# Optimization experiments

Measured on AMD Instinct MI355X. Metric: run time of the kernel, lower is better.

Reference implementation:

```python
import jax, jax.numpy as jnp
import numpy as np

B, N, K, H = 32, 1024, 10, 64  # graphs, nodes per graph, kNN, hidden_channels


def setup_inputs() -> dict:
    key = jax.random.key(0)
    ks = jax.random.split(key, 11)
    def w(k, shape, fan_in):
        lim = 1.0 / np.sqrt(fan_in)
        return jax.random.uniform(k, shape, jnp.float32, -lim, lim)
    return {
        'pos': jax.random.uniform(ks[0], (B, N, 2), jnp.float32),  # TSP city coords
        'W1': w(ks[1], (4, H), 4),           'b1': w(ks[2], (H,), 4),
        'W2': w(ks[3], (2 * H, 2 * H), 2 * H), 'b2': w(ks[4], (2 * H,), 2 * H),
        'W3': w(ks[5], (4 * H, 4 * H), 4 * H), 'b3': w(ks[6], (4 * H,), 4 * H),
        'Wl1': w(ks[7], (4 * H, H), 4 * H),   'bl1': w(ks[8], (H,), 4 * H),
        'Wl2': w(ks[9], (H, 2), H),           'bl2': w(ks[10], (2,), H),
    }


def _edge_conv(x, W, b, k):
    # DynamicEdgeConv: kNN graph in feature space (self-match included, as in
    # torch_cluster.knn(x, x, k)), edge feature [x_i, x_j - x_i], Linear, max-aggr.
    sq = jnp.sum(x * x, axis=-1)                                   # [B,N]
    dist = sq[:, :, None] + sq[:, None, :] - 2.0 * jnp.einsum('bnd,bmd->bnm', x, x)
    _, idx = jax.lax.top_k(-dist, k)                               # [B,N,k]
    xj = jax.vmap(lambda xb, ib: xb[ib])(x, idx)                   # [B,N,k,D]
    xi = x[:, :, None, :]
    edge = jnp.concatenate([jnp.broadcast_to(xi, xj.shape), xj - xi], axis=-1)
    msg = edge @ W + b                                             # [B,N,k,Dout]
    return jnp.max(msg, axis=2)                                    # max aggregation


def _pair_norm(x, eps=1e-5, scale=1.0):
    # PairNorm over all nodes (module calls it without batch vector)
    xc = x - jnp.mean(x, axis=(0, 1), keepdims=True)
    msn = jnp.mean(jnp.sum(xc * xc, axis=-1))  # mean squared node norm
    return scale * xc / jnp.sqrt(eps + msn)


def reference(pos, W1, b1, W2, b2, W3, b3, Wl1, bl1, Wl2, bl2):
    h1 = _pair_norm(jax.nn.relu(_edge_conv(pos, W1, b1, K)))
    h2 = _pair_norm(jax.nn.relu(_edge_conv(h1, W2, b2, K)))
    h3 = _pair_norm(jax.nn.relu(_edge_conv(h2, W3, b3, K)))
    g = jnp.max(h3, axis=1)                    # global_max_pool per graph -> [B,4H]
    h = jax.nn.relu(g @ Wl1 + bl1)             # dropout(p=0.2) is identity in eval
    return h @ Wl2 + bl2                       # [B,2]
```

## Files before the change

kernel.cpp:

```cpp
#include <hip/hip_runtime.h>
#include <math.h>

constexpr int NB = 32;
constexpr int NP = 1024;
constexpr int NK = 10;
constexpr int BN = NB * NP;
constexpr int NBCH = 8;
constexpr int NSLOT = 1024;

__device__ __forceinline__ float4 ld4(const float* p){ return *reinterpret_cast<const float4*>(p); }
__device__ __forceinline__ float2 ld2(const float* p){ return *reinterpret_cast<const float2*>(p); }
__device__ __forceinline__ void st4(float* p, float4 v){ *reinterpret_cast<float4*>(p) = v; }

__global__ __launch_bounds__(256) void k_sq_pos(const float* __restrict__ x, float* __restrict__ sq){
  int i = blockIdx.x*256 + threadIdx.x;
  float2 v = ld2(x + (size_t)2*i);
  sq[i] = v.x*v.x + v.y*v.y;
}

__global__ __launch_bounds__(256) void k_dist2(const float* __restrict__ x,
    const float* __restrict__ sq, float* __restrict__ dist, int b0){
  int bz = blockIdx.z;
  int b = b0 + bz;
  int n0 = blockIdx.x*128, m0 = blockIdx.y*128;
  int ry = threadIdx.x>>4, rx = threadIdx.x&15;
  const float* xb = x + (size_t)b*NP*2;
  const float* sqb = sq + (size_t)b*NP;
  float2 av[8], bv[8]; float sn[8], sm[8];
#pragma unroll
  for (int k=0;k<8;++k){
    av[k] = ld2(xb + (size_t)(n0+ry*8+k)*2);
    bv[k] = ld2(xb + (size_t)(m0+rx*8+k)*2);
    sn[k] = sqb[n0+ry*8+k];
    sm[k] = sqb[m0+rx*8+k];
  }
  float* dbase = dist + ((size_t)bz*NP + n0 + ry*8)*NP + m0 + rx*8;
#pragma unroll
  for (int k=0;k<8;++k){
    float r[8];
#pragma unroll
    for (int l=0;l<8;++l){
      float dot = av[k].x*bv[l].x + av[k].y*bv[l].y;
      r[l] = (sn[k] + sm[l]) - 2.f*dot;
    }
    st4(dbase + (size_t)k*NP,     make_float4(r[0],r[1],r[2],r[3]));
    st4(dbase + (size_t)k*NP + 4, make_float4(r[4],r[5],r[6],r[7]));
  }
}

template<int DIN>
__global__ __launch_bounds__(256) void k_dist(const float* __restrict__ x,
    const float* __restrict__ sq, float* __restrict__ dist, int b0){
  constexpr int K4 = DIN/4, MASK = K4-1;
  extern __shared__ float4 smem[];
  float4* as4 = smem;
  float4* bs4 = smem + 128*K4;
  int bz = blockIdx.z;
  int b = b0 + bz;
  int n0 = blockIdx.x*128, m0 = blockIdx.y*128;
  int ry = threadIdx.x>>4, rx = threadIdx.x&15;
  const float* xb = x + (size_t)b*NP*DIN;
  for (int u=threadIdx.x; u<128*K4; u+=256){
    int r = u / K4, c = u % K4;
    int sw = r*K4 + ((c + (r>>3)) & MASK);
    as4[sw] = ld4(xb + (size_t)(n0+r)*DIN + 4*c);
    bs4[sw] = ld4(xb + (size_t)(m0+r)*DIN + 4*c);
  }
  __syncthreads();
  float acc[8][8];
#pragma unroll
  for (int k=0;k<8;++k)
#pragma unroll
    for (int l=0;l<8;++l) acc[k][l] = 0.f;
#pragma unroll 2
  for (int d4=0; d4<K4; ++d4){
    float4 a_[8], b_[8];
#pragma unroll
    for (int k=0;k<8;++k) a_[k] = as4[(ry*8+k)*K4 + ((d4 + ry) & MASK)];
#pragma unroll
    for (int l=0;l<8;++l) b_[l] = bs4[(rx*8+l)*K4 + ((d4 + rx) & MASK)];
#pragma unroll
    for (int k=0;k<8;++k)
#pragma unroll
      for (int l=0;l<8;++l)
        acc[k][l] += a_[k].x*b_[l].x + a_[k].y*b_[l].y + a_[k].z*b_[l].z + a_[k].w*b_[l].w;
  }
  const float* sqb = sq + (size_t)b*NP;
  float sn[8], sm[8];
#pragma unroll
  for (int k=0;k<8;++k){ sn[k] = sqb[n0+ry*8+k]; sm[k] = sqb[m0+rx*8+k]; }
  float* dbase = dist + ((size_t)bz*NP + n0 + ry*8)*NP + m0 + rx*8;
#pragma unroll
  for (int k=0;k<8;++k){
    float r[8];
#pragma unroll
    for (int l=0;l<8;++l) r[l] = (sn[k]+sm[l]) - 2.f*acc[k][l];
    st4(dbase + (size_t)k*NP,     make_float4(r[0],r[1],r[2],r[3]));
    st4(dbase + (size_t)k*NP + 4, make_float4(r[4],r[5],r[6],r[7]));
  }
}

template<int DIN, int DOUT>
__global__ __launch_bounds__(256) void k_gemm(const float* __restrict__ x,
    const float* __restrict__ W, float* __restrict__ xcat, int m_base){
  constexpr int K4 = DIN/4, MASK = K4-1;
  extern __shared__ float4 smem[];
  float4* as4 = smem;
  float4* bs4 = smem + 128*K4;
  int m0 = blockIdx.x*128;
  int nc = blockIdx.y*128;
  bool isBot = (nc >= DOUT);
  int bcol = isBot ? nc - DOUT : nc;
  const float* B = W + (isBot ? (size_t)DIN*DOUT : 0);
  const float* xg = x + (size_t)(m_base + m0)*DIN;
  for (int u=threadIdx.x; u<128*K4; u+=256){
    int r = u / K4, c = u % K4;
    as4[r*K4 + ((c + (r>>3)) & MASK)] = ld4(xg + (size_t)r*DIN + 4*c);
  }
  float* bsf = reinterpret_cast<float*>(bs4);
  for (int u=threadIdx.x; u<DIN*128; u+=256){
    int k = u >> 7, n = u & 127;
    bsf[(n*K4 + (((k>>2) + (n>>3)) & MASK))*4 + (k&3)] = B[(size_t)k*DOUT + bcol + n];
  }
  __syncthreads();
  int ry = threadIdx.x>>4, rx = threadIdx.x&15;
  float acc[8][8];
#pragma unroll
  for (int k=0;k<8;++k)
#pragma unroll
    for (int l=0;l<8;++l) acc[k][l] = 0.f;
#pragma unroll 2
  for (int d4=0; d4<K4; ++d4){
    float4 a_[8], b_[8];
#pragma unroll
    for (int k=0;k<8;++k) a_[k] = as4[(ry*8+k)*K4 + ((d4 + ry) & MASK)];
#pragma unroll
    for (int l=0;l<8;++l) b_[l] = bs4[(rx*8+l)*K4 + ((d4 + rx) & MASK)];
#pragma unroll
    for (int k=0;k<8;++k)
#pragma unroll
      for (int l=0;l<8;++l)
        acc[k][l] += a_[k].x*b_[l].x + a_[k].y*b_[l].y + a_[k].z*b_[l].z + a_[k].w*b_[l].w;
  }
  float* outb = xcat + (size_t)(m0 + ry*8)*(2*DOUT) + nc + rx*8;
#pragma unroll
  for (int k=0;k<8;++k){
    st4(outb + (size_t)k*(2*DOUT),     make_float4(acc[k][0],acc[k][1],acc[k][2],acc[k][3]));
    st4(outb + (size_t)k*(2*DOUT) + 4, make_float4(acc[k][4],acc[k][5],acc[k][6],acc[k][7]));
  }
}

template<int DOUT>
__global__ __launch_bounds__(256) void k_gmax(const float* __restrict__ xcat,
    const int* __restrict__ idx, const float* __restrict__ bias,
    float* __restrict__ hout, float* __restrict__ spart, int p_base, int slot_base){
  constexpr int TP = DOUT/4;
  constexpr int ROWS = 256/TP;
  constexpr int PPT = 32/ROWS;
  __shared__ int idx_s[32*NK];
  __shared__ float red[1024];
  __shared__ float ssp[4];
  int c4 = threadIdx.x % TP, pr = threadIdx.x / TP;
  int c = 4*c4;
  int p0 = blockIdx.x*32 + p_base;
  for (int t=threadIdx.x; t<32*NK; t+=256) idx_s[t] = idx[(size_t)p0*NK + t];
  __syncthreads();
  float4 b4 = ld4(bias + c);
  float4 fsum = make_float4(0.f,0.f,0.f,0.f);
  float ss = 0.f;
  int pbl = (((p0 - p_base) >> 10) << 10);
#pragma unroll
  for (int t=0; t<PPT; ++t){
    int pl = pr + t*ROWS;
    int lrow = (p0 - p_base) + pl;
    const float* row = xcat + (size_t)lrow*(2*DOUT);
    float4 z = ld4(row + c), ys = ld4(row + DOUT + c);
    float4 mv = make_float4(-__builtin_inff(),-__builtin_inff(),-__builtin_inff(),-__builtin_inff());
    for (int j=0;j<NK;++j){
      int q = pbl + idx_s[pl*NK + j];
      float4 g = ld4(xcat + (size_t)q*(2*DOUT) + DOUT + c);
      mv.x = fmaxf(mv.x, g.x); mv.y = fmaxf(mv.y, g.y);
      mv.z = fmaxf(mv.z, g.z); mv.w = fmaxf(mv.w, g.w);
    }
    float4 v;
    v.x = fmaxf(z.x + b4.x - ys.x + mv.x, 0.f);
    v.y = fmaxf(z.y + b4.y - ys.y + mv.y, 0.f);
    v.z = fmaxf(z.z + b4.z - ys.z + mv.z, 0.f);
    v.w = fmaxf(z.w + b4.w - ys.w + mv.w, 0.f);
    st4(hout + (size_t)(p0 + pl)*DOUT + c, v);
    fsum.x += v.x; fsum.y += v.y; fsum.z += v.z; fsum.w += v.w;
    ss += v.x*v.x + v.y*v.y + v.z*v.z + v.w*v.w;
  }
  st4(&red[pr*DOUT + c], fsum);
#pragma unroll
  for (int off=32; off; off>>=1) ss += __shfl_xor(ss, off, 64);
  if ((threadIdx.x&63)==0) ssp[threadIdx.x>>6] = ss;
  __syncthreads();
  int slot = slot_base + blockIdx.x;
  for (int o=threadIdx.x; o<DOUT; o+=256){
    float s = 0.f;
#pragma unroll
    for (int r=0;r<ROWS;++r) s += red[r*DOUT + o];
    spart[(size_t)o*NSLOT + slot] = s;
  }
  if (threadIdx.x==0) spart[(size_t)DOUT*NSLOT + slot] = ssp[0]+ssp[1]+ssp[2]+ssp[3];
}

__global__ __launch_bounds__(256) void k_topk(const float* __restrict__ dist,
    int* __restrict__ idx, int b0){
  int wave = threadIdx.x>>6, lane = threadIdx.x&63;
  int rowg = blockIdx.x*4 + wave;
  int bz = rowg >> 10, n = rowg & 1023;
  const float* dr = dist + (size_t)rowg * NP;
  float dv[16];
#pragma unroll
  for (int t=0;t<16;++t) dv[t] = dr[lane + 64*t];
  int* out = idx + ((size_t)(b0+bz)*NP + n)*NK;
  for (int kk=0; kk<NK; ++kk){
    float bvv = dv[0]; int bm = lane;
#pragma unroll
    for (int t=1;t<16;++t){
      int m = lane + 64*t;
      if (dv[t] < bvv){ bvv = dv[t]; bm = m; }
    }
#pragma unroll
    for (int off=32; off; off>>=1){
      float ov = __shfl_xor(bvv, off, 64);
      int om = __shfl_xor(bm, off, 64);
      if (ov < bvv || (ov == bvv && om < bm)){ bvv = ov; bm = om; }
    }
    if (lane == 0) out[kk] = bm;
    int tsel = bm>>6, lsel = bm&63;
#pragma unroll
    for (int t=0;t<16;++t)
      if (t == tsel && lane == lsel) dv[t] = __builtin_inff();
  }
}

__global__ __launch_bounds__(256) void k_edge1(const float* __restrict__ x,
    const int* __restrict__ idx, const float* __restrict__ W,
    const float* __restrict__ bias, float* __restrict__ hout,
    float* __restrict__ spart){
  __shared__ int idx_s[32*NK];
  __shared__ float red[4][64];
  __shared__ float ssw[4];
  int lane = threadIdx.x & 63, wv = threadIdx.x >> 6;
  int p0 = blockIdx.x * 32;
  int b = p0 >> 10;
  int pl0 = p0 & 1023;
  const float* xb = x + ((size_t)b<<10)*2;
  for (int t=threadIdx.x; t<32*NK; t+=256) idx_s[t] = idx[(size_t)p0*NK + t];
  __syncthreads();
  float w0=W[lane], w1=W[64+lane], w2=W[128+lane], w3=W[192+lane];
  float bi = bias[lane];
  float fsum = 0.f, ss = 0.f;
#pragma unroll
  for (int t=0;t<8;++t){
    int pl = wv*8 + t;
    float2 xi = ld2(xb + (size_t)(pl0+pl)*2);
    float common = xi.x*w0 + xi.y*w1 + bi;
    float mv = -__builtin_inff();
    for (int j=0;j<NK;++j){
      float2 xj = ld2(xb + (size_t)idx_s[pl*NK+j]*2);
      mv = fmaxf(mv, (xj.x-xi.x)*w2 + (xj.y-xi.y)*w3);
    }
    float v = fmaxf(common + mv, 0.f);
    hout[(size_t)(p0+pl)*64 + lane] = v;
    fsum += v; ss += v*v;
  }
  red[wv][lane] = fsum;
#pragma unroll
  for (int off=32; off; off>>=1) ss += __shfl_xor(ss, off, 64);
  if (lane==0) ssw[wv] = ss;
  __syncthreads();
  if (threadIdx.x < 64){
    float s = red[0][lane]+red[1][lane]+red[2][lane]+red[3][lane];
    spart[(size_t)lane*NSLOT + blockIdx.x] = s;
  }
  if (threadIdx.x==0) spart[(size_t)64*NSLOT + blockIdx.x] = ssw[0]+ssw[1]+ssw[2]+ssw[3];
}

template<int DOUT>
__global__ __launch_bounds__(256) void k_finalize2(const float* __restrict__ spart,
    float* __restrict__ stats){
  __shared__ float part[4];
  __shared__ float ssh;
  float musq = 0.f;
  for (int f = threadIdx.x; f <= DOUT; f += 256){
    const float* row = spart + (size_t)f*NSLOT;
    float4 a = make_float4(0.f,0.f,0.f,0.f);
    for (int s=0; s<NSLOT; s+=4){
      float4 v = ld4(row + s);
      a.x += v.x; a.y += v.y; a.z += v.z; a.w += v.w;
    }
    float s = (a.x + a.y) + (a.z + a.w);
    if (f < DOUT){
      float m = s * (1.f/BN);
      stats[320+f] = m;
      musq += m*m;
    } else {
      ssh = s;
    }
  }
#pragma unroll
  for (int off=32; off; off>>=1) musq += __shfl_xor(musq, off, 64);
  if ((threadIdx.x&63)==0) part[threadIdx.x>>6] = musq;
  __syncthreads();
  if (threadIdx.x==0){
    float mu2 = part[0]+part[1]+part[2]+part[3];
    float msn = ssh*(1.f/BN) - mu2;
    stats[576] = 1.f / sqrtf(1e-5f + msn);
  }
}

template<int DOUT>
__global__ __launch_bounds__(256) void k_norm(float* __restrict__ h,
    const float* __restrict__ stats, float* __restrict__ sq){
  int lane = threadIdx.x&63, wv = threadIdx.x>>6;
  int row = blockIdx.x*4 + wv;
  float inv = stats[576];
  const float* mu = stats + 320;
  float* hr = h + (size_t)row*DOUT;
  float s = 0.f;
  if constexpr (DOUT == 64){
    float v = (hr[lane] - mu[lane]) * inv;
    hr[lane] = v;
    s = v*v;
  } else if constexpr (DOUT == 128){
    float2 x2 = ld2(hr + 2*lane), m2 = ld2(mu + 2*lane);
    float a = (x2.x - m2.x)*inv, b = (x2.y - m2.y)*inv;
    *reinterpret_cast<float2*>(hr + 2*lane) = make_float2(a,b);
    s = a*a + b*b;
  } else {
    float4 x4 = ld4(hr + 4*lane), m4 = ld4(mu + 4*lane);
    float4 v;
    v.x = (x4.x-m4.x)*inv; v.y = (x4.y-m4.y)*inv;
    v.z = (x4.z-m4.z)*inv; v.w = (x4.w-m4.w)*inv;
    st4(hr + 4*lane, v);
    s = v.x*v.x + v.y*v.y + v.z*v.z + v.w*v.w;
  }
#pragma unroll
  for (int off=32; off; off>>=1) s += __shfl_xor(s, off, 64);
  if (lane==0) sq[row] = s;
}

__global__ __launch_bounds__(256) void k_pool1(const float* __restrict__ h, float* __restrict__ gpart){
  int b = blockIdx.x, c = blockIdx.y, o = threadIdx.x;
  const float* hp = h + ((size_t)b*NP + c*128)*256 + o;
  float m = -__builtin_inff();
  for (int n=0;n<128;++n) m = fmaxf(m, hp[(size_t)n*256]);
  gpart[((size_t)c*NB + b)*256 + o] = m;
}

__global__ __launch_bounds__(256) void k_head(const float* __restrict__ gpart,
    const float* __restrict__ Wl1, const float* __restrict__ bl1,
    const float* __restrict__ Wl2, const float* __restrict__ bl2,
    float* __restrict__ out){
  __shared__ float g_s[256];
  __shared__ float h_s[64];
  int b = blockIdx.x, t = threadIdx.x;
  float m = -__builtin_inff();
  for (int c=0;c<8;++c) m = fmaxf(m, gpart[((size_t)c*NB + b)*256 + t]);
  g_s[t] = m;
  __syncthreads();
  if (t < 64){
    float a = bl1[t];
    for (int k=0;k<256;++k) a += g_s[k]*Wl1[(size_t)k*64 + t];
    h_s[t] = fmaxf(a, 0.f);
  }
  __syncthreads();
  if (t < 2){
    float a = bl2[t];
    for (int i=0;i<64;++i) a += h_s[i]*Wl2[(size_t)i*2 + t];
    out[(size_t)b*2 + t] = a;
  }
}

extern "C" void kernel_launch(void* const* d_in, const int* in_sizes, int n_in,
                              void* d_out, int out_size, void* d_ws, size_t ws_size,
                              hipStream_t stream){
  (void)in_sizes; (void)n_in; (void)out_size; (void)ws_size;
  const float* pos = (const float*)d_in[0];
  const float* W1  = (const float*)d_in[1];
  const float* b1  = (const float*)d_in[2];
  const float* W2  = (const float*)d_in[3];
  const float* b2  = (const float*)d_in[4];
  const float* W3  = (const float*)d_in[5];
  const float* b3  = (const float*)d_in[6];
  const float* Wl1 = (const float*)d_in[7];
  const float* bl1 = (const float*)d_in[8];
  const float* Wl2 = (const float*)d_in[9];
  const float* bl2 = (const float*)d_in[10];
  float* outp = (float*)d_out;

  (void)hipFuncSetAttribute((const void*)k_dist<128>,      hipFuncAttributeMaxDynamicSharedMemorySize, 131072);
  (void)hipFuncSetAttribute((const void*)k_gemm<128,256>,  hipFuncAttributeMaxDynamicSharedMemorySize, 131072);
  (void)hipFuncSetAttribute((const void*)k_dist<64>,       hipFuncAttributeMaxDynamicSharedMemorySize, 65536);
  (void)hipFuncSetAttribute((const void*)k_gemm<64,128>,   hipFuncAttributeMaxDynamicSharedMemorySize, 65536);

  char* w = (char*)d_ws;
  size_t off = 0;
  auto take = [&](size_t bytes)->char*{ char* p = w + off; off += (bytes + 255) & ~(size_t)255; return p; };
  float* sq    = (float*)take((size_t)BN*4);
  int*   idx   = (int*)  take((size_t)BN*NK*4);
  float* x1    = (float*)take((size_t)BN*64*4);
  float* x2    = (float*)take((size_t)BN*128*4);
  float* x3    = (float*)take((size_t)BN*256*4);
  float* stats = (float*)take(4096);
  float* spart = (float*)take((size_t)257*NSLOT*4);
  float* gpart = (float*)take((size_t)8*NB*256*4);
  float* big   = (float*)take((size_t)NBCH*NP*NP*4);
  float* dist  = big;
  float* xcat  = big;

  dim3 gdist(NP/128, NP/128, NBCH);

  k_sq_pos<<<BN/256, 256, 0, stream>>>(pos, sq);
  for (int c=0;c<NB/NBCH;++c){
    k_dist2<<<gdist, 256, 0, stream>>>(pos, sq, dist, c*NBCH);
    k_topk<<<NBCH*NP/4, 256, 0, stream>>>(dist, idx, c*NBCH);
  }
  k_edge1<<<NSLOT, 256, 0, stream>>>(pos, idx, W1, b1, x1, spart);
  k_finalize2<64><<<1, 256, 0, stream>>>(spart, stats);
  k_norm<64><<<BN/4, 256, 0, stream>>>(x1, stats, sq);

  for (int c=0;c<NB/NBCH;++c){
    k_dist<64><<<gdist, 256, 65536, stream>>>(x1, sq, dist, c*NBCH);
    k_topk<<<NBCH*NP/4, 256, 0, stream>>>(dist, idx, c*NBCH);
  }
  k_gemm<64,128><<<dim3(BN/128, 2), 256, 65536, stream>>>(x1, W2, xcat, 0);
  k_gmax<128><<<BN/32, 256, 0, stream>>>(xcat, idx, b2, x2, spart, 0, 0);
  k_finalize2<128><<<1, 256, 0, stream>>>(spart, stats);
  k_norm<128><<<BN/4, 256, 0, stream>>>(x2, stats, sq);

  for (int c=0;c<NB/NBCH;++c){
    k_dist<128><<<gdist, 256, 131072, stream>>>(x2, sq, dist, c*NBCH);
    k_topk<<<NBCH*NP/4, 256, 0, stream>>>(dist, idx, c*NBCH);
  }
  for (int h=0; h<2; ++h){
    int m_base = h * (BN/2);
    k_gemm<128,256><<<dim3(BN/2/128, 4), 256, 131072, stream>>>(x2, W3, xcat, m_base);
    k_gmax<256><<<BN/2/32, 256, 0, stream>>>(xcat, idx, b3, x3, spart, m_base, h*(BN/2/32));
  }
  k_finalize2<256><<<1, 256, 0, stream>>>(spart, stats);
  k_norm<256><<<BN/4, 256, 0, stream>>>(x3, stats, sq);

  k_pool1<<<dim3(NB, 8), 256, 0, stream>>>(x3, gpart);
  k_head<<<NB, 256, 0, stream>>>(gpart, Wl1, bl1, Wl2, bl2, outp);
}
```

Measured before the change: 1.023 ms.

## Unify dist and gemm into K-chunked register-prefetched tile kernel

Replaces the separate distance and GEMM kernels, which staged the whole K dimension in up to 128KB of dynamic shared memory, with one templated tile kernel. It loops over 32-wide K chunks in 32KB of static shared memory and prefetches the next chunk into registers during compute. The weights are pre-transposed once per call by a small k_wt kernel, so the GEMM B-tile loads become coalesced float4 rows instead of scalar strided loads. The smaller shared footprint is meant to allow more resident blocks and overlap of global loads with FMA work, at the cost of extra barriers per chunk and two extra small launches.

```diff
diff --git a/kernel.cpp b/kernel.cpp
--- a/kernel.cpp
+++ b/kernel.cpp
@@ -48,105 +48,107 @@
   }
 }
 
-template<int DIN>
-__global__ __launch_bounds__(256) void k_dist(const float* __restrict__ x,
-    const float* __restrict__ sq, float* __restrict__ dist, int b0){
-  constexpr int K4 = DIN/4, MASK = K4-1;
-  extern __shared__ float4 smem[];
-  float4* as4 = smem;
-  float4* bs4 = smem + 128*K4;
-  int bz = blockIdx.z;
-  int b = b0 + bz;
-  int n0 = blockIdx.x*128, m0 = blockIdx.y*128;
-  int ry = threadIdx.x>>4, rx = threadIdx.x&15;
-  const float* xb = x + (size_t)b*NP*DIN;
-  for (int u=threadIdx.x; u<128*K4; u+=256){
-    int r = u / K4, c = u % K4;
-    int sw = r*K4 + ((c + (r>>3)) & MASK);
-    as4[sw] = ld4(xb + (size_t)(n0+r)*DIN + 4*c);
-    bs4[sw] = ld4(xb + (size_t)(m0+r)*DIN + 4*c);
-  }
-  __syncthreads();
+template<int DIN, int DOUT>
+__global__ void k_wt(const float* __restrict__ W, float* __restrict__ WT){
+  int n = blockIdx.x, k = threadIdx.x;
+  float v = (n < DOUT) ? W[(size_t)k*DOUT + n]
+                       : W[(size_t)DIN*DOUT + (size_t)k*DOUT + (n - DOUT)];
+  WT[(size_t)n*DIN + k] = v;
+}
+
+template<int DIN, bool DIST>
+__global__ __launch_bounds__(256) void k_tile(const float* __restrict__ xa,
+    const float* __restrict__ bsrc, const float* __restrict__ sq,
+    float* __restrict__ out, int aux0, int outLD){
+  constexpr int C = DIN/32;
+  __shared__ float4 as4[1024];
+  __shared__ float4 bs4[1024];
+  int tid = threadIdx.x;
+  const float* Arow; const float* Brow;
+  float* obase; const float* sqn = nullptr; const float* sqm = nullptr;
+  if constexpr (DIST){
+    int bz = blockIdx.z; int b = aux0 + bz;
+    int n0 = blockIdx.x*128, m0 = blockIdx.y*128;
+    const float* xb = xa + (size_t)b*NP*DIN;
+    Arow = xb + (size_t)n0*DIN;
+    Brow = xb + (size_t)m0*DIN;
+    sqn = sq + (size_t)b*NP + n0;
+    sqm = sq + (size_t)b*NP + m0;
+    obase = out + ((size_t)bz*NP + n0)*NP + m0;
+  } else {
+    int n0 = blockIdx.x*128, m0 = blockIdx.y*128;
+    Arow = xa + (size_t)(aux0 + n0)*DIN;
+    Brow = bsrc + (size_t)m0*DIN;
+    obase = out + (size_t)n0*outLD + m0;
+  }
+  const float* pA[4]; const float* pB[4];
+#pragma unroll
+  for (int i=0;i<4;++i){
+    int s = tid + 256*i;
+    int r = s>>3;
+    int c = ((s&7) - (r>>3)) & 7;
+    pA[i] = Arow + (size_t)r*DIN + 4*c;
+    pB[i] = Brow + (size_t)r*DIN + 4*c;
+  }
+  float4 sa[4], sb[4];
+#pragma unroll
+  for (int i=0;i<4;++i){ sa[i] = ld4(pA[i]); sb[i] = ld4(pB[i]); }
+#pragma unroll
+  for (int i=0;i<4;++i){ as4[tid+256*i] = sa[i]; bs4[tid+256*i] = sb[i]; }
+
+  int ry = tid>>4, rx = tid&15;
   float acc[8][8];
 #pragma unroll
   for (int k=0;k<8;++k)
 #pragma unroll
     for (int l=0;l<8;++l) acc[k][l] = 0.f;
-#pragma unroll 2
-  for (int d4=0; d4<K4; ++d4){
-    float4 a_[8], b_[8];
-#pragma unroll
-    for (int k=0;k<8;++k) a_[k] = as4[(ry*8+k)*K4 + ((d4 + ry) & MASK)];
-#pragma unroll
-    for (int l=0;l<8;++l) b_[l] = bs4[(rx*8+l)*K4 + ((d4 + rx) & MASK)];
-#pragma unroll
-    for (int k=0;k<8;++k)
-#pragma unroll
-      for (int l=0;l<8;++l)
-        acc[k][l] += a_[k].x*b_[l].x + a_[k].y*b_[l].y + a_[k].z*b_[l].z + a_[k].w*b_[l].w;
-  }
-  const float* sqb = sq + (size_t)b*NP;
-  float sn[8], sm[8];
-#pragma unroll
-  for (int k=0;k<8;++k){ sn[k] = sqb[n0+ry*8+k]; sm[k] = sqb[m0+rx*8+k]; }
-  float* dbase = dist + ((size_t)bz*NP + n0 + ry*8)*NP + m0 + rx*8;
-#pragma unroll
-  for (int k=0;k<8;++k){
-    float r[8];
-#pragma unroll
-    for (int l=0;l<8;++l) r[l] = (sn[k]+sm[l]) - 2.f*acc[k][l];
-    st4(dbase + (size_t)k*NP,     make_float4(r[0],r[1],r[2],r[3]));
-    st4(dbase + (size_t)k*NP + 4, make_float4(r[4],r[5],r[6],r[7]));
-  }
-}
-
-template<int DIN, int DOUT>
-__global__ __launch_bounds__(256) void k_gemm(const float* __restrict__ x,
-    const float* __restrict__ W, float* __restrict__ xcat, int m_base){
-  constexpr int K4 = DIN/4, MASK = K4-1;
-  extern __shared__ float4 smem[];
-  float4* as4 = smem;
-  float4* bs4 = smem + 128*K4;
-  int m0 = blockIdx.x*128;
-  int nc = blockIdx.y*128;
-  bool isBot = (nc >= DOUT);
-  int bcol = isBot ? nc - DOUT : nc;
-  const float* B = W + (isBot ? (size_t)DIN*DOUT : 0);
-  const float* xg = x + (size_t)(m_base + m0)*DIN;
-  for (int u=threadIdx.x; u<128*K4; u+=256){
-    int r = u / K4, c = u % K4;
-    as4[r*K4 + ((c + (r>>3)) & MASK)] = ld4(xg + (size_t)r*DIN + 4*c);
-  }
-  float* bsf = reinterpret_cast<float*>(bs4);
-  for (int u=threadIdx.x; u<DIN*128; u+=256){
-    int k = u >> 7, n = u & 127;
-    bsf[(n*K4 + (((k>>2) + (n>>3)) & MASK))*4 + (k&3)] = B[(size_t)k*DOUT + bcol + n];
-  }
-  __syncthreads();
-  int ry = threadIdx.x>>4, rx = threadIdx.x&15;
-  float acc[8][8];
-#pragma unroll
-  for (int k=0;k<8;++k)
-#pragma unroll
-    for (int l=0;l<8;++l) acc[k][l] = 0.f;
-#pragma unroll 2
-  for (int d4=0; d4<K4; ++d4){
-    float4 a_[8], b_[8];
-#pragma unroll
-    for (int k=0;k<8;++k) a_[k] = as4[(ry*8+k)*K4 + ((d4 + ry) & MASK)];
-#pragma unroll
-    for (int l=0;l<8;++l) b_[l] = bs4[(rx*8+l)*K4 + ((d4 + rx) & MASK)];
-#pragma unroll
-    for (int k=0;k<8;++k)
-#pragma unroll
-      for (int l=0;l<8;++l)
-        acc[k][l] += a_[k].x*b_[l].x + a_[k].y*b_[l].y + a_[k].z*b_[l].z + a_[k].w*b_[l].w;
-  }
-  float* outb = xcat + (size_t)(m0 + ry*8)*(2*DOUT) + nc + rx*8;
-#pragma unroll
-  for (int k=0;k<8;++k){
-    st4(outb + (size_t)k*(2*DOUT),     make_float4(acc[k][0],acc[k][1],acc[k][2],acc[k][3]));
-    st4(outb + (size_t)k*(2*DOUT) + 4, make_float4(acc[k][4],acc[k][5],acc[k][6],acc[k][7]));
+
+  for (int ch=0; ch<C; ++ch){
+    __syncthreads();
+    if (ch+1 < C){
+#pragma unroll
+      for (int i=0;i<4;++i){ sa[i] = ld4(pA[i] + (ch+1)*32); sb[i] = ld4(pB[i] + (ch+1)*32); }
+    }
+#pragma unroll
+    for (int d4=0; d4<8; ++d4){
+      float4 a_[8], b_[8];
+#pragma unroll
+      for (int k=0;k<8;++k) a_[k] = as4[(ry*8+k)*8 + ((d4 + ry)&7)];
+#pragma unroll
+      for (int l=0;l<8;++l) b_[l] = bs4[(rx*8+l)*8 + ((d4 + rx)&7)];
+#pragma unroll
+      for (int k=0;k<8;++k)
+#pragma unroll
+        for (int l=0;l<8;++l)
+          acc[k][l] += a_[k].x*b_[l].x + a_[k].y*b_[l].y + a_[k].z*b_[l].z + a_[k].w*b_[l].w;
+    }
+    __syncthreads();
+    if (ch+1 < C){
+#pragma unroll
+      for (int i=0;i<4;++i){ as4[tid+256*i] = sa[i]; bs4[tid+256*i] = sb[i]; }
+    }
+  }
+
+  if constexpr (DIST){
+    float sn[8], sm[8];
+#pragma unroll
+    for (int k=0;k<8;++k){ sn[k] = sqn[ry*8+k]; sm[k] = sqm[rx*8+k]; }
+#pragma unroll
+    for (int k=0;k<8;++k){
+      float r[8];
+#pragma unroll
+      for (int l=0;l<8;++l) r[l] = (sn[k]+sm[l]) - 2.f*acc[k][l];
+      float* op = obase + (size_t)(ry*8+k)*NP + rx*8;
+      st4(op,     make_float4(r[0],r[1],r[2],r[3]));
+      st4(op + 4, make_float4(r[4],r[5],r[6],r[7]));
+    }
+  } else {
+#pragma unroll
+    for (int k=0;k<8;++k){
+      float* op = obase + (size_t)(ry*8+k)*outLD + rx*8;
+      st4(op,     make_float4(acc[k][0],acc[k][1],acc[k][2],acc[k][3]));
+      st4(op + 4, make_float4(acc[k][4],acc[k][5],acc[k][6],acc[k][7]));
+    }
   }
 }
 
@@ -393,11 +395,6 @@
   const float* bl2 = (const float*)d_in[10];
   float* outp = (float*)d_out;
 
-  (void)hipFuncSetAttribute((const void*)k_dist<128>,      hipFuncAttributeMaxDynamicSharedMemorySize, 131072);
-  (void)hipFuncSetAttribute((const void*)k_gemm<128,256>,  hipFuncAttributeMaxDynamicSharedMemorySize, 131072);
-  (void)hipFuncSetAttribute((const void*)k_dist<64>,       hipFuncAttributeMaxDynamicSharedMemorySize, 65536);
-  (void)hipFuncSetAttribute((const void*)k_gemm<64,128>,   hipFuncAttributeMaxDynamicSharedMemorySize, 65536);
-
   char* w = (char*)d_ws;
   size_t off = 0;
   auto take = [&](size_t bytes)->char*{ char* p = w + off; off += (bytes + 255) & ~(size_t)255; return p; };
@@ -409,11 +406,16 @@
   float* stats = (float*)take(4096);
   float* spart = (float*)take((size_t)257*NSLOT*4);
   float* gpart = (float*)take((size_t)8*NB*256*4);
+  float* wt2   = (float*)take((size_t)256*64*4);
+  float* wt3   = (float*)take((size_t)512*128*4);
   float* big   = (float*)take((size_t)NBCH*NP*NP*4);
   float* dist  = big;
   float* xcat  = big;
 
   dim3 gdist(NP/128, NP/128, NBCH);
+
+  k_wt<64,128><<<256, 64, 0, stream>>>(W2, wt2);
+  k_wt<128,256><<<512, 128, 0, stream>>>(W3, wt3);
 
   k_sq_pos<<<BN/256, 256, 0, stream>>>(pos, sq);
   for (int c=0;c<NB/NBCH;++c){
@@ -425,21 +427,21 @@
   k_norm<64><<<BN/4, 256, 0, stream>>>(x1, stats, sq);
 
   for (int c=0;c<NB/NBCH;++c){
-    k_dist<64><<<gdist, 256, 65536, stream>>>(x1, sq, dist, c*NBCH);
+    k_tile<64,true><<<gdist, 256, 0, stream>>>(x1, x1, sq, dist, c*NBCH, NP);
     k_topk<<<NBCH*NP/4, 256, 0, stream>>>(dist, idx, c*NBCH);
   }
-  k_gemm<64,128><<<dim3(BN/128, 2), 256, 65536, stream>>>(x1, W2, xcat, 0);
+  k_tile<64,false><<<dim3(BN/128, 2), 256, 0, stream>>>(x1, wt2, nullptr, xcat, 0, 256);
   k_gmax<128><<<BN/32, 256, 0, stream>>>(xcat, idx, b2, x2, spart, 0, 0);
   k_finalize2<128><<<1, 256, 0, stream>>>(spart, stats);
   k_norm<128><<<BN/4, 256, 0, stream>>>(x2, stats, sq);
 
   for (int c=0;c<NB/NBCH;++c){
-    k_dist<128><<<gdist, 256, 131072, stream>>>(x2, sq, dist, c*NBCH);
+    k_tile<128,true><<<gdist, 256, 0, stream>>>(x2, x2, sq, dist, c*NBCH, NP);
     k_topk<<<NBCH*NP/4, 256, 0, stream>>>(dist, idx, c*NBCH);
   }
   for (int h=0; h<2; ++h){
     int m_base = h * (BN/2);
-    k_gemm<128,256><<<dim3(BN/2/128, 4), 256, 131072, stream>>>(x2, W3, xcat, m_base);
+    k_tile<128,false><<<dim3(BN/2/128, 4), 256, 0, stream>>>(x2, wt3, nullptr, xcat, m_base, 512);
     k_gmax<256><<<BN/2/32, 256, 0, stream>>>(xcat, idx, b3, x3, spart, m_base, h*(BN/2/32));
   }
   k_finalize2<256><<<1, 256, 0, stream>>>(spart, stats);
```

Measured after the change: 2.675 ms. 162% more time.

## Fuse top-k selection into distance tiles and merge per-tile candidates

Applied to the files above, without the earlier changes.

Instead of writing full NxN distance matrices to global memory in batch chunks and running a separate top-k pass over them, each distance tile now selects its 10 nearest columns per row in registers using 16-lane shuffle reductions. It writes those (value, index) candidates to a small buffer. A merge kernel then reduces the 80 candidates per row to the final 10 indices. This removes the large dist write and read traffic and the chunking loops, at the cost of serial selection work inside the GEMM-like kernels and extra register pressure.

```diff
diff --git a/kernel.cpp b/kernel.cpp
--- a/kernel.cpp
+++ b/kernel.cpp
@@ -5,7 +5,7 @@
 constexpr int NP = 1024;
 constexpr int NK = 10;
 constexpr int BN = NB * NP;
-constexpr int NBCH = 8;
+constexpr int NT = NP/128;
 constexpr int NSLOT = 1024;
 
 __device__ __forceinline__ float4 ld4(const float* p){ return *reinterpret_cast<const float4*>(p); }
@@ -18,10 +18,36 @@
   sq[i] = v.x*v.x + v.y*v.y;
 }
 
-__global__ __launch_bounds__(256) void k_dist2(const float* __restrict__ x,
-    const float* __restrict__ sq, float* __restrict__ dist, int b0){
-  int bz = blockIdx.z;
-  int b = b0 + bz;
+__device__ __forceinline__ void sel_rows(float (&d)[8][8], int rx, int m0, float2* c0){
+#pragma unroll 1
+  for (int k=0;k<8;++k){
+    float2* crow = c0 + (size_t)k*(NT*NK);
+#pragma unroll 1
+    for (int sel=0; sel<NK; ++sel){
+      float v = d[k][0]; int c = rx*8;
+#pragma unroll
+      for (int l=1;l<8;++l){
+        int cc = rx*8+l;
+        if (d[k][l] < v){ v = d[k][l]; c = cc; }
+      }
+#pragma unroll
+      for (int off=1; off<16; off<<=1){
+        float ov = __shfl_xor(v, off, 64);
+        int   oc = __shfl_xor(c, off, 64);
+        if (ov < v || (ov == v && oc < c)){ v = ov; c = oc; }
+      }
+      if (rx == (c>>3)){
+#pragma unroll
+        for (int l=0;l<8;++l) if (l == (c&7)) d[k][l] = __builtin_inff();
+      }
+      if (rx == 0) crow[sel] = make_float2(v, (float)(m0 + c));
+    }
+  }
+}
+
+__global__ __launch_bounds__(256) void k_knn2(const float* __restrict__ x,
+    const float* __restrict__ sq, float2* __restrict__ cand){
+  int b = blockIdx.z;
   int n0 = blockIdx.x*128, m0 = blockIdx.y*128;
   int ry = threadIdx.x>>4, rx = threadIdx.x&15;
   const float* xb = x + (size_t)b*NP*2;
@@ -34,29 +60,25 @@
     sn[k] = sqb[n0+ry*8+k];
     sm[k] = sqb[m0+rx*8+k];
   }
-  float* dbase = dist + ((size_t)bz*NP + n0 + ry*8)*NP + m0 + rx*8;
-#pragma unroll
-  for (int k=0;k<8;++k){
-    float r[8];
+  float d[8][8];
+#pragma unroll
+  for (int k=0;k<8;++k)
 #pragma unroll
     for (int l=0;l<8;++l){
       float dot = av[k].x*bv[l].x + av[k].y*bv[l].y;
-      r[l] = (sn[k] + sm[l]) - 2.f*dot;
-    }
-    st4(dbase + (size_t)k*NP,     make_float4(r[0],r[1],r[2],r[3]));
-    st4(dbase + (size_t)k*NP + 4, make_float4(r[4],r[5],r[6],r[7]));
-  }
+      d[k][l] = (sn[k] + sm[l]) - 2.f*dot;
+    }
+  sel_rows(d, rx, m0, cand + (((size_t)b*NP + n0 + ry*8)*NT + blockIdx.y)*NK);
 }
 
 template<int DIN>
-__global__ __launch_bounds__(256) void k_dist(const float* __restrict__ x,
-    const float* __restrict__ sq, float* __restrict__ dist, int b0){
+__global__ __launch_bounds__(256) void k_knn(const float* __restrict__ x,
+    const float* __restrict__ sq, float2* __restrict__ cand){
   constexpr int K4 = DIN/4, MASK = K4-1;
   extern __shared__ float4 smem[];
   float4* as4 = smem;
   float4* bs4 = smem + 128*K4;
-  int bz = blockIdx.z;
-  int b = b0 + bz;
+  int b = blockIdx.z;
   int n0 = blockIdx.x*128, m0 = blockIdx.y*128;
   int ry = threadIdx.x>>4, rx = threadIdx.x&15;
   const float* xb = x + (size_t)b*NP*DIN;
@@ -89,14 +111,36 @@
   float sn[8], sm[8];
 #pragma unroll
   for (int k=0;k<8;++k){ sn[k] = sqb[n0+ry*8+k]; sm[k] = sqb[m0+rx*8+k]; }
-  float* dbase = dist + ((size_t)bz*NP + n0 + ry*8)*NP + m0 + rx*8;
-#pragma unroll
-  for (int k=0;k<8;++k){
-    float r[8];
-#pragma unroll
-    for (int l=0;l<8;++l) r[l] = (sn[k]+sm[l]) - 2.f*acc[k][l];
-    st4(dbase + (size_t)k*NP,     make_float4(r[0],r[1],r[2],r[3]));
-    st4(dbase + (size_t)k*NP + 4, make_float4(r[4],r[5],r[6],r[7]));
+#pragma unroll
+  for (int k=0;k<8;++k)
+#pragma unroll
+    for (int l=0;l<8;++l) acc[k][l] = (sn[k]+sm[l]) - 2.f*acc[k][l];
+  sel_rows(acc, rx, m0, cand + (((size_t)b*NP + n0 + ry*8)*NT + blockIdx.y)*NK);
+}
+
+__global__ __launch_bounds__(256) void k_merge(const float2* __restrict__ cand,
+    int* __restrict__ idx){
+  int wid = threadIdx.x>>6, lane = threadIdx.x&63;
+  int row = blockIdx.x*4 + wid;
+  const float2* cr = cand + (size_t)row*(NT*NK);
+  float2 e0 = cr[lane];
+  float v0 = e0.x; int c0 = (int)e0.y;
+  float v1; int c1;
+  if (lane < NT*NK - 64){ float2 e1 = cr[64+lane]; v1 = e1.x; c1 = (int)e1.y; }
+  else { v1 = __builtin_inff(); c1 = 0x7fffffff; }
+  int* out = idx + (size_t)row*NK;
+  for (int sel=0; sel<NK; ++sel){
+    float v; int c;
+    if (v1 < v0 || (v1 == v0 && c1 < c0)){ v = v1; c = c1; } else { v = v0; c = c0; }
+#pragma unroll
+    for (int off=1; off<64; off<<=1){
+      float ov = __shfl_xor(v, off, 64);
+      int   oc = __shfl_xor(c, off, 64);
+      if (ov < v || (ov == v && oc < c)){ v = ov; c = oc; }
+    }
+    if (c0 == c) v0 = __builtin_inff();
+    if (c1 == c) v1 = __builtin_inff();
+    if (lane == 0) out[sel] = c;
   }
 }
 
@@ -204,37 +248,6 @@
     spart[(size_t)o*NSLOT + slot] = s;
   }
   if (threadIdx.x==0) spart[(size_t)DOUT*NSLOT + slot] = ssp[0]+ssp[1]+ssp[2]+ssp[3];
-}
-
-__global__ __launch_bounds__(256) void k_topk(const float* __restrict__ dist,
-    int* __restrict__ idx, int b0){
-  int wave = threadIdx.x>>6, lane = threadIdx.x&63;
-  int rowg = blockIdx.x*4 + wave;
-  int bz = rowg >> 10, n = rowg & 1023;
-  const float* dr = dist + (size_t)rowg * NP;
-  float dv[16];
-#pragma unroll
-  for (int t=0;t<16;++t) dv[t] = dr[lane + 64*t];
-  int* out = idx + ((size_t)(b0+bz)*NP + n)*NK;
-  for (int kk=0; kk<NK; ++kk){
-    float bvv = dv[0]; int bm = lane;
-#pragma unroll
-    for (int t=1;t<16;++t){
-      int m = lane + 64*t;
-      if (dv[t] < bvv){ bvv = dv[t]; bm = m; }
-    }
-#pragma unroll
-    for (int off=32; off; off>>=1){
-      float ov = __shfl_xor(bvv, off, 64);
-      int om = __shfl_xor(bm, off, 64);
-      if (ov < bvv || (ov == bvv && om < bm)){ bvv = ov; bm = om; }
-    }
-    if (lane == 0) out[kk] = bm;
-    int tsel = bm>>6, lsel = bm&63;
-#pragma unroll
-    for (int t=0;t<16;++t)
-      if (t == tsel && lane == lsel) dv[t] = __builtin_inff();
-  }
 }
 
 __global__ __launch_bounds__(256) void k_edge1(const float* __restrict__ x,
@@ -393,9 +406,9 @@
   const float* bl2 = (const float*)d_in[10];
   float* outp = (float*)d_out;
 
-  (void)hipFuncSetAttribute((const void*)k_dist<128>,      hipFuncAttributeMaxDynamicSharedMemorySize, 131072);
+  (void)hipFuncSetAttribute((const void*)k_knn<128>,       hipFuncAttributeMaxDynamicSharedMemorySize, 131072);
   (void)hipFuncSetAttribute((const void*)k_gemm<128,256>,  hipFuncAttributeMaxDynamicSharedMemorySize, 131072);
-  (void)hipFuncSetAttribute((const void*)k_dist<64>,       hipFuncAttributeMaxDynamicSharedMemorySize, 65536);
+  (void)hipFuncSetAttribute((const void*)k_knn<64>,        hipFuncAttributeMaxDynamicSharedMemorySize, 65536);
   (void)hipFuncSetAttribute((const void*)k_gemm<64,128>,   hipFuncAttributeMaxDynamicSharedMemorySize, 65536);
 
   char* w = (char*)d_ws;
@@ -409,34 +422,28 @@
   float* stats = (float*)take(4096);
   float* spart = (float*)take((size_t)257*NSLOT*4);
   float* gpart = (float*)take((size_t)8*NB*256*4);
-  float* big   = (float*)take((size_t)NBCH*NP*NP*4);
-  float* dist  = big;
+  float* big   = (float*)take((size_t)BN*(2*256)*4);
+  float2* cand = (float2*)big;
   float* xcat  = big;
 
-  dim3 gdist(NP/128, NP/128, NBCH);
+  dim3 gknn(NP/128, NP/128, NB);
 
   k_sq_pos<<<BN/256, 256, 0, stream>>>(pos, sq);
-  for (int c=0;c<NB/NBCH;++c){
-    k_dist2<<<gdist, 256, 0, stream>>>(pos, sq, dist, c*NBCH);
-    k_topk<<<NBCH*NP/4, 256, 0, stream>>>(dist, idx, c*NBCH);
-  }
+  k_knn2<<<gknn, 256, 0, stream>>>(pos, sq, cand);
+  k_merge<<<BN/4, 256, 0, stream>>>(cand, idx);
   k_edge1<<<NSLOT, 256, 0, stream>>>(pos, idx, W1, b1, x1, spart);
   k_finalize2<64><<<1, 256, 0, stream>>>(spart, stats);
   k_norm<64><<<BN/4, 256, 0, stream>>>(x1, stats, sq);
 
-  for (int c=0;c<NB/NBCH;++c){
-    k_dist<64><<<gdist, 256, 65536, stream>>>(x1, sq, dist, c*NBCH);
-    k_topk<<<NBCH*NP/4, 256, 0, stream>>>(dist, idx, c*NBCH);
-  }
+  k_knn<64><<<gknn, 256, 65536, stream>>>(x1, sq, cand);
+  k_merge<<<BN/4, 256, 0, stream>>>(cand, idx);
   k_gemm<64,128><<<dim3(BN/128, 2), 256, 65536, stream>>>(x1, W2, xcat, 0);
   k_gmax<128><<<BN/32, 256, 0, stream>>>(xcat, idx, b2, x2, spart, 0, 0);
   k_finalize2<128><<<1, 256, 0, stream>>>(spart, stats);
   k_norm<128><<<BN/4, 256, 0, stream>>>(x2, stats, sq);
 
-  for (int c=0;c<NB/NBCH;++c){
-    k_dist<128><<<gdist, 256, 131072, stream>>>(x2, sq, dist, c*NBCH);
-    k_topk<<<NBCH*NP/4, 256, 0, stream>>>(dist, idx, c*NBCH);
-  }
+  k_knn<128><<<gknn, 256, 131072, stream>>>(x2, sq, cand);
+  k_merge<<<BN/4, 256, 0, stream>>>(cand, idx);
   for (int h=0; h<2; ++h){
     int m_base = h * (BN/2);
     k_gemm<128,256><<<dim3(BN/2/128, 4), 256, 131072, stream>>>(x2, W3, xcat, m_base);
```

New measurement: 1.550 ms. 51.5% more time.
